# Kernel tuning notes

Measured on AMD Instinct MI355X. Metric: run time of the kernel, lower is better.

## Reference

```python
import jax, jax.numpy as jnp
import numpy as np

INNER = 64  # hardcoded inner_dim in the torch module


def _knn_idx(pos, k):
    # dgcnn-style knn: topk of negative squared distance (includes self)
    d2 = jnp.sum(pos * pos, axis=-1)                      # (b, n)
    sim = 2.0 * jnp.einsum('bic,bjc->bij', pos, pos) - d2[:, :, None] - d2[:, None, :]
    return jax.lax.top_k(sim, k)[1]                       # (b, n, k)


def setup_inputs() -> dict:
    key = jax.random.key(0)
    ks = jax.random.split(key, 16)
    emb_dim = 256
    b, n, k = 8, 2048, 16
    s = 0.05
    inp = {
        'x': jax.random.normal(ks[0], (b, n, emb_dim), dtype=jnp.float32),
        'pos': jax.random.normal(ks[1], (b, n, 3), dtype=jnp.float32),
        'w_qkv': jax.random.normal(ks[2], (emb_dim, 3 * INNER), dtype=jnp.float32) * s,
        'w_pos1': jax.random.normal(ks[3], (3, 64), dtype=jnp.float32) * s,
        'b_pos1': jnp.zeros((64,), dtype=jnp.float32),
        'w_pos2': jax.random.normal(ks[4], (64, INNER), dtype=jnp.float32) * s,
        'b_pos2': jnp.zeros((INNER,), dtype=jnp.float32),
        'w_att1': jax.random.normal(ks[5], (INNER, 4 * INNER), dtype=jnp.float32) * s,
        'b_att1': jnp.zeros((4 * INNER,), dtype=jnp.float32),
        'w_att2': jax.random.normal(ks[6], (4 * INNER, INNER), dtype=jnp.float32) * s,
        'b_att2': jnp.zeros((INNER,), dtype=jnp.float32),
        'w_out': jax.random.normal(ks[7], (INNER, emb_dim), dtype=jnp.float32) * s,
        'b_out': jnp.zeros((emb_dim,), dtype=jnp.float32),
        'k': k,
    }
    return inp


def reference(x, pos, w_qkv, w_pos1, b_pos1, w_pos2, b_pos2,
              w_att1, b_att1, w_att2, b_att2, w_out, b_out, k):
    b, n, _ = x.shape
    qkv = x @ w_qkv                                        # (b, n, 3*INNER)
    q, kk, v = jnp.split(qkv, 3, axis=-1)                  # each (b, n, INNER)

    idx = _knn_idx(pos, k) + (jnp.arange(b) * n)[:, None, None]  # flat offsets
    idxf = idx.reshape(-1)

    def gather(t, d):
        return jnp.take(t.reshape(b * n, d), idxf, axis=0).reshape(b, n, k, d)

    pos_nn = gather(pos, 3)                                # (b, n, k, 3)
    rel_pos = pos_nn - pos[:, :, None, :]
    rpe = jax.nn.relu(rel_pos @ w_pos1 + b_pos1) @ w_pos2 + b_pos2  # (b, n, k, INNER)

    q_nn = gather(q, INNER)
    k_nn = gather(kk, INNER)
    v_nn = gather(v, INNER) + rpe

    h = q_nn - k_nn + rpe
    sim = jax.nn.relu(h @ w_att1 + b_att1) @ w_att2 + b_att2       # (b, n, k, INNER)

    # NOTE: faithful to torch source — softmax over the CHANNEL dim (-1),
    # then L2-normalize over the neighbor dim (-2).
    attn = jax.nn.softmax(sim, axis=-1)
    norm = jnp.sqrt(jnp.sum(attn * attn, axis=-2, keepdims=True))
    attn = attn / jnp.maximum(norm, 1e-12)

    agg = jnp.sum(attn * v_nn, axis=2)                     # (b, n, INNER)
    return agg @ w_out + b_out                             # (b, n, emb_dim)
```

## Files before the change

### kernel.cpp

```cpp
#include <hip/hip_runtime.h>
#include <stdint.h>

typedef __attribute__((ext_vector_type(8))) short bf8v;
typedef __attribute__((ext_vector_type(4))) float f4v;
typedef __attribute__((ext_vector_type(4))) unsigned int u4v;
typedef __attribute__((ext_vector_type(2))) unsigned int u2v;

#define MFMA16(a,b,c) __builtin_amdgcn_mfma_f32_16x16x32_bf16((a),(b),(c),0,0,0)

__device__ __forceinline__ unsigned short f2bf(float f) {
    unsigned u = __float_as_uint(f);
    return (unsigned short)((u + 0x7FFFu + ((u >> 16) & 1u)) >> 16);
}
#define SW(row,k,L) ((row)*(L) + ((k) ^ (((row)&7)<<3)))

#define WS_QMK   0u
#define WS_V     4194304u
#define WS_AGG   8388608u
#define WS_IDX   12582912u
#define WS_W1T   13631488u
#define WS_W2T   13664256u
#define WS_WPT   13697024u
#define WS_WQK   13705216u
#define WS_WOUT  13770752u

__global__ __launch_bounds__(256) void k_prep(
    const float* __restrict__ w_qkv, const float* __restrict__ w_pos2,
    const float* __restrict__ w_att1, const float* __restrict__ w_att2,
    const float* __restrict__ w_out, char* __restrict__ ws)
{
    int t = blockIdx.x * 256 + threadIdx.x;
    unsigned short* w1i = (unsigned short*)(ws + WS_W1T);
    unsigned short* w2i = (unsigned short*)(ws + WS_W2T);
    unsigned short* wpi = (unsigned short*)(ws + WS_WPT);
    unsigned short* wqi = (unsigned short*)(ws + WS_WQK);
    unsigned short* woi = (unsigned short*)(ws + WS_WOUT);
    if (t < 16384) {
        int hid = t >> 6, k = t & 63;
        w1i[hid*64 + (k ^ ((hid&7)<<3))] = f2bf(w_att1[k*256 + hid]);
    } else if (t < 32768) {
        int i = t - 16384; int ch = i >> 8, k = i & 255;
        w2i[ch*256 + (k ^ ((ch&7)<<3))] = f2bf(w_att2[k*64 + ch]);
    } else if (t < 36864) {
        int i = t - 32768; int ch = i >> 6, k = i & 63;
        wpi[ch*64 + (k ^ ((ch&7)<<3))] = f2bf(w_pos2[k*64 + ch]);
    } else if (t < 69632) {
        int i = t - 36864; int col = i >> 8, k = i & 255;
        float val = (col < 64) ? (w_qkv[k*192 + col] - w_qkv[k*192 + 64 + col])
                               : w_qkv[k*192 + 128 + (col - 64)];
        wqi[col*256 + (k ^ ((col&7)<<3))] = f2bf(val);
    } else if (t < 86016) {
        int i = t - 69632; int col = i >> 6, k = i & 63;
        woi[col*64 + (k ^ ((col&7)<<3))] = f2bf(w_out[k*256 + col]);
    }
}

__global__ __launch_bounds__(256) void k_knn(const float* __restrict__ pos,
                                             int* __restrict__ idxo) {
    const int wid = threadIdx.x >> 6, lane = threadIdx.x & 63;
    const int pid = blockIdx.x * 4 + wid;
    const int b = pid >> 11, i = pid & 2047;
    const float* pb = pos + (size_t)b * 2048 * 3;
    float xi = pb[i*3], yi = pb[i*3+1], zi = pb[i*3+2];
    float d2i = xi*xi; d2i = fmaf(yi, yi, d2i); d2i = fmaf(zi, zi, d2i);
    unsigned long long key[32];
#pragma unroll
    for (int m = 0; m < 32; ++m) {
        int j = m * 64 + lane;
        float xj = pb[j*3], yj = pb[j*3+1], zj = pb[j*3+2];
        float d2j = xj*xj; d2j = fmaf(yj, yj, d2j); d2j = fmaf(zj, zj, d2j);
        float dot = xi*xj; dot = fmaf(yi, yj, dot); dot = fmaf(zi, zj, dot);
        float sim = 2.0f*dot - d2i - d2j;
        unsigned u = __float_as_uint(sim);
        unsigned fk = (u & 0x80000000u) ? ~u : (u | 0x80000000u);
        key[m] = ((unsigned long long)fk << 32) | (unsigned)(0xFFFFFFFFu - (unsigned)j);
    }
    unsigned long long lmax = key[0];
#pragma unroll
    for (int m = 1; m < 32; ++m) lmax = (key[m] > lmax) ? key[m] : lmax;
    int my = 0;
    for (int it = 0; it < 16; ++it) {
        unsigned long long wmax = lmax;
#pragma unroll
        for (int st = 32; st >= 1; st >>= 1) {
            unsigned long long o = __shfl_xor(wmax, st);
            wmax = (o > wmax) ? o : wmax;
        }
        int jw = (int)(0xFFFFFFFFu - (unsigned)(wmax & 0xFFFFFFFFull));
        if (lane == it) my = jw;
        if (lmax == wmax) {
#pragma unroll
            for (int m = 0; m < 32; ++m) if (key[m] == wmax) key[m] = 0ull;
            lmax = key[0];
#pragma unroll
            for (int m = 1; m < 32; ++m) lmax = (key[m] > lmax) ? key[m] : lmax;
        }
    }
    if (lane < 16) idxo[pid * 16 + lane] = b * 2048 + my;
}

__global__ __launch_bounds__(256, 1) void k_qkv(const float* __restrict__ x,
        const char* __restrict__ wimg, float* __restrict__ qmk, float* __restrict__ v) {
    extern __shared__ char smem[];
    unsigned short* WQ = (unsigned short*)smem;
    unsigned short* XT = (unsigned short*)(smem + 65536);
    const int tid = threadIdx.x, wid = tid >> 6, lane = tid & 63;
    const int q4 = lane >> 4, l15 = lane & 15;
#pragma unroll
    for (int itn = 0; itn < 16; ++itn) {
        int off = itn * 4096 + tid * 16;
        *(u4v*)(smem + off) = *(const u4v*)(wimg + off);
    }
    __syncthreads();
    {
        int r = tid >> 2, k64 = (tid & 3) * 64;
        const float* xr = x + ((size_t)blockIdx.x * 64 + r) * 256 + k64;
#pragma unroll
        for (int c = 0; c < 8; ++c) {
            f4v a = *(const f4v*)(xr + c*8);
            f4v bq = *(const f4v*)(xr + c*8 + 4);
            bf8v s;
            s[0]=(short)f2bf(a[0]); s[1]=(short)f2bf(a[1]); s[2]=(short)f2bf(a[2]); s[3]=(short)f2bf(a[3]);
            s[4]=(short)f2bf(bq[0]); s[5]=(short)f2bf(bq[1]); s[6]=(short)f2bf(bq[2]); s[7]=(short)f2bf(bq[3]);
            *(bf8v*)&XT[SW(r, k64 + c*8, 256)] = s;
        }
    }
    f4v z = {0.f,0.f,0.f,0.f};
    f4v acc[8];
#pragma unroll
    for (int n = 0; n < 8; ++n) acc[n] = z;
    const int arow = wid*16 + l15;
#pragma unroll
    for (int ks = 0; ks < 8; ++ks) {
        int k0 = ks*32 + q4*8;
        bf8v a = *(const bf8v*)&XT[SW(arow, k0, 256)];
#pragma unroll
        for (int nt = 0; nt < 8; ++nt) {
            bf8v bq = *(const bf8v*)&WQ[SW(nt*16 + l15, k0, 256)];
            acc[nt] = MFMA16(a, bq, acc[nt]);
        }
    }
    size_t rbase = (size_t)blockIdx.x * 64 + wid*16 + q4*4;
#pragma unroll
    for (int nt = 0; nt < 8; ++nt) {
        int col = nt*16 + l15;
#pragma unroll
        for (int j = 0; j < 4; ++j) {
            if (nt < 4) qmk[(rbase + j)*64 + col] = acc[nt][j];
            else        v[(rbase + j)*64 + (col - 64)] = acc[nt][j];
        }
    }
}

__global__ __launch_bounds__(256, 1) void k_att(
    const float* __restrict__ qmk, const float* __restrict__ v,
    const float* __restrict__ pos, const int* __restrict__ idx,
    const float* __restrict__ w_pos1, const float* __restrict__ b_pos1,
    const float* __restrict__ b_pos2, const float* __restrict__ b_att1,
    const float* __restrict__ b_att2, const char* __restrict__ wblob,
    float* __restrict__ agg)
{
    extern __shared__ char smem[];
    unsigned short* W1T = (unsigned short*)smem;
    unsigned short* W2T = (unsigned short*)(smem + 32768);
    unsigned short* WPT = (unsigned short*)(smem + 65536);
    const int tid = threadIdx.x, wid = tid >> 6, lane = tid & 63;
    const int q4 = lane >> 4, l15 = lane & 15;
    char* wb = smem + 73728 + wid * 16640;
    unsigned short* PH = (unsigned short*)wb;
    unsigned short* H  = (unsigned short*)(wb + 2048);
    float*          RV = (float*)(wb + 4096);
    unsigned short* C1 = (unsigned short*)(wb + 8448);

#pragma unroll
    for (int itn = 0; itn < 18; ++itn) {
        int off = itn * 4096 + tid * 16;
        *(u4v*)(smem + off) = *(const u4v*)(wblob + off);
    }
    __syncthreads();

    float bp2[16], ba2[16];
#pragma unroll
    for (int mt = 0; mt < 4; ++mt)
#pragma unroll
        for (int j = 0; j < 4; ++j) {
            int ch = mt*16 + q4*4 + j;
            bp2[mt*4+j] = b_pos2[ch];
            ba2[mt*4+j] = b_att2[ch];
        }

    const int r4 = lane >> 2, c16 = (lane & 3) * 16;
    f4v z = {0.f,0.f,0.f,0.f};

    for (int it = 0; it < 16; ++it) {
        const int point = (blockIdx.x * 4 + wid) * 16 + it;
        {
            int grow = point * 16 + r4;
            int flat = idx[grow];
            float cx = pos[point*3], cy = pos[point*3+1], cz = pos[point*3+2];
            float r0 = pos[flat*3] - cx, r1 = pos[flat*3+1] - cy, r2 = pos[flat*3+2] - cz;
            bf8v lo, hi;
#pragma unroll
            for (int i = 0; i < 16; ++i) {
                int h = c16 + i;
                float t = fmaf(r2, w_pos1[128+h], fmaf(r1, w_pos1[64+h], fmaf(r0, w_pos1[h], b_pos1[h])));
                t = fmaxf(t, 0.f);
                if (i < 8) lo[i] = (short)f2bf(t); else hi[i-8] = (short)f2bf(t);
            }
            *(bf8v*)&PH[SW(r4, c16, 64)] = lo;
            *(bf8v*)&PH[SW(r4, c16+8, 64)] = hi;
        }
        {
            f4v ga[4];
#pragma unroll
            for (int mt = 0; mt < 4; ++mt) ga[mt] = z;
#pragma unroll
            for (int ks = 0; ks < 2; ++ks) {
                int k0 = ks*32 + q4*8;
                bf8v bfr = *(const bf8v*)&PH[SW(l15, k0, 64)];
#pragma unroll
                for (int mt = 0; mt < 4; ++mt)
                    ga[mt] = MFMA16(*(const bf8v*)&WPT[SW(mt*16 + l15, k0, 64)], bfr, ga[mt]);
            }
#pragma unroll
            for (int mt = 0; mt < 4; ++mt) {
                f4v o;
#pragma unroll
                for (int j = 0; j < 4; ++j) o[j] = ga[mt][j] + bp2[mt*4+j];
                *(f4v*)&RV[l15*68 + mt*16 + q4*4] = o;
            }
        }
        {
            int grow = point * 16 + r4;
            int flat = idx[grow];
            f4v rp[4], qk[4];
#pragma unroll
            for (int i = 0; i < 4; ++i) rp[i] = *(const f4v*)&RV[r4*68 + c16 + i*4];
#pragma unroll
            for (int i = 0; i < 4; ++i) qk[i] = *(const f4v*)(qmk + (size_t)flat*64 + c16 + i*4);
            bf8v lo, hi;
#pragma unroll
            for (int i = 0; i < 16; ++i) {
                float hv = rp[i>>2][i&3] + qk[i>>2][i&3];
                if (i < 8) lo[i] = (short)f2bf(hv); else hi[i-8] = (short)f2bf(hv);
            }
            *(bf8v*)&H[SW(r4, c16, 64)] = lo;
            *(bf8v*)&H[SW(r4, c16+8, 64)] = hi;
#pragma unroll
            for (int i = 0; i < 4; ++i) {
                f4v vv = *(const f4v*)(v + (size_t)flat*64 + c16 + i*4);
                f4v o;
#pragma unroll
                for (int j = 0; j < 4; ++j) o[j] = vv[j] + rp[i][j];
                *(f4v*)&RV[r4*68 + c16 + i*4] = o;
            }
        }
        {
            f4v cc[16];
#pragma unroll
            for (int mt = 0; mt < 16; ++mt) cc[mt] = z;
#pragma unroll
            for (int ks = 0; ks < 2; ++ks) {
                int k0 = ks*32 + q4*8;
                bf8v bfr = *(const bf8v*)&H[SW(l15, k0, 64)];
#pragma unroll
                for (int mt = 0; mt < 16; ++mt)
                    cc[mt] = MFMA16(*(const bf8v*)&W1T[SW(mt*16 + l15, k0, 64)], bfr, cc[mt]);
            }
#pragma unroll
            for (int mt = 0; mt < 16; ++mt) {
                f4v ba = *(const f4v*)(b_att1 + mt*16 + q4*4);
                float t0 = fmaxf(cc[mt][0]+ba[0], 0.f), t1 = fmaxf(cc[mt][1]+ba[1], 0.f);
                float t2 = fmaxf(cc[mt][2]+ba[2], 0.f), t3 = fmaxf(cc[mt][3]+ba[3], 0.f);
                u2v pp;
                pp[0] = (unsigned)f2bf(t0) | ((unsigned)f2bf(t1) << 16);
                pp[1] = (unsigned)f2bf(t2) | ((unsigned)f2bf(t3) << 16);
                *(u2v*)&C1[SW(l15, mt*16 + q4*4, 256)] = pp;
            }
        }
        {
            f4v ss[4];
#pragma unroll
            for (int mt = 0; mt < 4; ++mt) ss[mt] = z;
#pragma unroll
            for (int ks = 0; ks < 8; ++ks) {
                int k0 = ks*32 + q4*8;
                bf8v bfr = *(const bf8v*)&C1[SW(l15, k0, 256)];
#pragma unroll
                for (int mt = 0; mt < 4; ++mt)
                    ss[mt] = MFMA16(*(const bf8v*)&W2T[SW(mt*16 + l15, k0, 256)], bfr, ss[mt]);
            }
            float e[16];
            float mx = -3.4e38f;
#pragma unroll
            for (int i = 0; i < 16; ++i) { e[i] = ss[i>>2][i&3] + ba2[i]; mx = fmaxf(mx, e[i]); }
            mx = fmaxf(mx, __shfl_xor(mx, 16));
            mx = fmaxf(mx, __shfl_xor(mx, 32));
            float sum = 0.f;
#pragma unroll
            for (int i = 0; i < 16; ++i) { e[i] = __expf(e[i] - mx); sum += e[i]; }
            sum += __shfl_xor(sum, 16);
            sum += __shfl_xor(sum, 32);
            float inv = 1.0f / sum;
            float nn[16];
#pragma unroll
            for (int i = 0; i < 16; ++i) { e[i] *= inv; nn[i] = e[i]*e[i]; }
#pragma unroll
            for (int st = 1; st <= 8; st <<= 1)
#pragma unroll
                for (int i = 0; i < 16; ++i) nn[i] += __shfl_xor(nn[i], st);
            float ag[16];
#pragma unroll
            for (int mt = 0; mt < 4; ++mt) {
                f4v vn = *(const f4v*)&RV[l15*68 + mt*16 + q4*4];
#pragma unroll
                for (int j = 0; j < 4; ++j) {
                    int i = mt*4 + j;
                    float a = e[i] / fmaxf(sqrtf(nn[i]), 1e-12f);
                    ag[i] = a * vn[j];
                }
            }
#pragma unroll
            for (int st = 1; st <= 8; st <<= 1)
#pragma unroll
                for (int i = 0; i < 16; ++i) ag[i] += __shfl_xor(ag[i], st);
            if (l15 == 0) {
#pragma unroll
                for (int mt = 0; mt < 4; ++mt) {
                    f4v o;
#pragma unroll
                    for (int j = 0; j < 4; ++j) o[j] = ag[mt*4+j];
                    *(f4v*)(agg + (size_t)point*64 + mt*16 + q4*4) = o;
                }
            }
        }
    }
}

__global__ __launch_bounds__(256, 1) void k_out(const float* __restrict__ agg,
        const char* __restrict__ wimg, const float* __restrict__ b_out,
        float* __restrict__ outp) {
    extern __shared__ char smem[];
    unsigned short* WO = (unsigned short*)smem;
    unsigned short* AT = (unsigned short*)(smem + 32768);
    const int tid = threadIdx.x, wid = tid >> 6, lane = tid & 63;
    const int q4 = lane >> 4, l15 = lane & 15;
#pragma unroll
    for (int itn = 0; itn < 8; ++itn) {
        int off = itn * 4096 + tid * 16;
        *(u4v*)(smem + off) = *(const u4v*)(wimg + off);
    }
    __syncthreads();
    {
        int r = tid >> 2, k16 = (tid & 3) * 16;
        const float* ar = agg + ((size_t)blockIdx.x * 64 + r) * 64 + k16;
        bf8v lo, hi;
#pragma unroll
        for (int i = 0; i < 16; ++i) {
            float t = ar[i];
            if (i < 8) lo[i] = (short)f2bf(t); else hi[i-8] = (short)f2bf(t);
        }
        *(bf8v*)&AT[SW(r, k16, 64)] = lo;
        *(bf8v*)&AT[SW(r, k16+8, 64)] = hi;
    }
    f4v z = {0.f,0.f,0.f,0.f};
    f4v acc[16];
#pragma unroll
    for (int nt = 0; nt < 16; ++nt) acc[nt] = z;
#pragma unroll
    for (int ks = 0; ks < 2; ++ks) {
        int k0 = ks*32 + q4*8;
        bf8v a = *(const bf8v*)&AT[SW(wid*16 + l15, k0, 64)];
#pragma unroll
        for (int nt = 0; nt < 16; ++nt) {
            bf8v bq = *(const bf8v*)&WO[SW(nt*16 + l15, k0, 64)];
            acc[nt] = MFMA16(a, bq, acc[nt]);
        }
    }
    size_t rbase = (size_t)blockIdx.x * 64 + wid*16 + q4*4;
#pragma unroll
    for (int nt = 0; nt < 16; ++nt) {
        int col = nt*16 + l15;
        float bo = b_out[col];
#pragma unroll
        for (int j = 0; j < 4; ++j)
            outp[(rbase + j)*256 + col] = acc[nt][j] + bo;
    }
}

extern "C" void kernel_launch(void* const* d_in, const int* in_sizes, int n_in,
                              void* d_out, int out_size, void* d_ws, size_t ws_size,
                              hipStream_t stream) {
    (void)in_sizes; (void)n_in; (void)out_size; (void)ws_size;
    const float* x      = (const float*)d_in[0];
    const float* pos    = (const float*)d_in[1];
    const float* w_qkv  = (const float*)d_in[2];
    const float* w_pos1 = (const float*)d_in[3];
    const float* b_pos1 = (const float*)d_in[4];
    const float* w_pos2 = (const float*)d_in[5];
    const float* b_pos2 = (const float*)d_in[6];
    const float* w_att1 = (const float*)d_in[7];
    const float* b_att1 = (const float*)d_in[8];
    const float* w_att2 = (const float*)d_in[9];
    const float* b_att2 = (const float*)d_in[10];
    const float* w_out  = (const float*)d_in[11];
    const float* b_out  = (const float*)d_in[12];
    float* outp = (float*)d_out;

    char* ws = (char*)d_ws;
    float* qmk = (float*)(ws + WS_QMK);
    float* v   = (float*)(ws + WS_V);
    float* agg = (float*)(ws + WS_AGG);
    int*   idx = (int*)(ws + WS_IDX);

    k_prep<<<dim3(336), dim3(256), 0, stream>>>(w_qkv, w_pos2, w_att1, w_att2, w_out, ws);
    k_knn<<<dim3(4096), dim3(256), 0, stream>>>(pos, idx);
    k_qkv<<<dim3(256), dim3(256), 98304, stream>>>(x, ws + WS_WQK, qmk, v);
    k_att<<<dim3(256), dim3(256), 140288, stream>>>(qmk, v, pos, idx,
                                                    w_pos1, b_pos1, b_pos2, b_att1, b_att2,
                                                    ws + WS_W1T, agg);
    k_out<<<dim3(256), dim3(256), 40960, stream>>>(agg, ws + WS_WOUT, b_out, outp);
}
```

Baseline: 591.8 us.

## Restructure attention kernel to keep rpe/v in registers and use 8 waves per block

```diff
diff --git a/kernel.cpp b/kernel.cpp
--- a/kernel.cpp
+++ b/kernel.cpp
@@ -152,7 +152,7 @@
     }
 }
 
-__global__ __launch_bounds__(256, 1) void k_att(
+__global__ __launch_bounds__(512, 2) void k_att(
     const float* __restrict__ qmk, const float* __restrict__ v,
     const float* __restrict__ pos, const int* __restrict__ idx,
     const float* __restrict__ w_pos1, const float* __restrict__ b_pos1,
@@ -166,172 +166,148 @@
     unsigned short* WPT = (unsigned short*)(smem + 65536);
     const int tid = threadIdx.x, wid = tid >> 6, lane = tid & 63;
     const int q4 = lane >> 4, l15 = lane & 15;
-    char* wb = smem + 73728 + wid * 16640;
+    const int r4 = lane >> 2, c16 = (lane & 3) * 16;
+    char* wb = smem + 73728 + wid * 10240;
+    unsigned short* P  = (unsigned short*)wb;
     unsigned short* PH = (unsigned short*)wb;
-    unsigned short* H  = (unsigned short*)(wb + 2048);
-    float*          RV = (float*)(wb + 4096);
-    unsigned short* C1 = (unsigned short*)(wb + 8448);
-
-#pragma unroll
-    for (int itn = 0; itn < 18; ++itn) {
-        int off = itn * 4096 + tid * 16;
+    unsigned short* H  = (unsigned short*)(wb + 8192);
+
+#pragma unroll
+    for (int it = 0; it < 9; ++it) {
+        int off = it * 8192 + tid * 16;
         *(u4v*)(smem + off) = *(const u4v*)(wblob + off);
     }
     __syncthreads();
 
-    float bp2[16], ba2[16];
-#pragma unroll
-    for (int mt = 0; mt < 4; ++mt)
-#pragma unroll
-        for (int j = 0; j < 4; ++j) {
-            int ch = mt*16 + q4*4 + j;
-            bp2[mt*4+j] = b_pos2[ch];
-            ba2[mt*4+j] = b_att2[ch];
-        }
-
-    const int r4 = lane >> 2, c16 = (lane & 3) * 16;
-    f4v z = {0.f,0.f,0.f,0.f};
-
-    for (int it = 0; it < 16; ++it) {
-        const int point = (blockIdx.x * 4 + wid) * 16 + it;
+#pragma unroll 1
+    for (int g = 0; g < 8; ++g) {
+        const int p = (blockIdx.x * 8 + wid) * 8 + g;
+        const int rowbase = p * 16;
+
+        const int flat_l = idx[rowbase + l15];
+        f4v qk[4], vv[4];
+#pragma unroll
+        for (int mt = 0; mt < 4; ++mt)
+            qk[mt] = *(const f4v*)(qmk + (size_t)flat_l * 64 + mt*16 + q4*4);
+#pragma unroll
+        for (int mt = 0; mt < 4; ++mt)
+            vv[mt] = *(const f4v*)(v + (size_t)flat_l * 64 + mt*16 + q4*4);
+
         {
-            int grow = point * 16 + r4;
-            int flat = idx[grow];
-            float cx = pos[point*3], cy = pos[point*3+1], cz = pos[point*3+2];
-            float r0 = pos[flat*3] - cx, r1 = pos[flat*3+1] - cy, r2 = pos[flat*3+2] - cz;
+            int flat_r = idx[rowbase + r4];
+            float cx = pos[p*3], cy = pos[p*3+1], cz = pos[p*3+2];
+            float r0 = pos[flat_r*3] - cx, r1 = pos[flat_r*3+1] - cy, r2v = pos[flat_r*3+2] - cz;
             bf8v lo, hi;
 #pragma unroll
-            for (int i = 0; i < 16; ++i) {
-                int h = c16 + i;
-                float t = fmaf(r2, w_pos1[128+h], fmaf(r1, w_pos1[64+h], fmaf(r0, w_pos1[h], b_pos1[h])));
-                t = fmaxf(t, 0.f);
-                if (i < 8) lo[i] = (short)f2bf(t); else hi[i-8] = (short)f2bf(t);
+            for (int u = 0; u < 4; ++u) {
+                f4v w0 = *(const f4v*)(w_pos1 + c16 + u*4);
+                f4v w1 = *(const f4v*)(w_pos1 + 64 + c16 + u*4);
+                f4v w2 = *(const f4v*)(w_pos1 + 128 + c16 + u*4);
+                f4v bb = *(const f4v*)(b_pos1 + c16 + u*4);
+#pragma unroll
+                for (int j = 0; j < 4; ++j) {
+                    float t = fmaf(r2v, w2[j], fmaf(r1, w1[j], fmaf(r0, w0[j], bb[j])));
+                    t = fmaxf(t, 0.f);
+                    if (u < 2) lo[u*4+j] = (short)f2bf(t);
+                    else       hi[(u-2)*4+j] = (short)f2bf(t);
+                }
             }
             *(bf8v*)&PH[SW(r4, c16, 64)] = lo;
             *(bf8v*)&PH[SW(r4, c16+8, 64)] = hi;
         }
-        {
-            f4v ga[4];
-#pragma unroll
-            for (int mt = 0; mt < 4; ++mt) ga[mt] = z;
-#pragma unroll
-            for (int ks = 0; ks < 2; ++ks) {
-                int k0 = ks*32 + q4*8;
-                bf8v bfr = *(const bf8v*)&PH[SW(l15, k0, 64)];
-#pragma unroll
-                for (int mt = 0; mt < 4; ++mt)
-                    ga[mt] = MFMA16(*(const bf8v*)&WPT[SW(mt*16 + l15, k0, 64)], bfr, ga[mt]);
+
+        f4v rp[4];
+#pragma unroll
+        for (int mt = 0; mt < 4; ++mt) rp[mt] = *(const f4v*)(b_pos2 + mt*16 + q4*4);
+#pragma unroll
+        for (int ks = 0; ks < 2; ++ks) {
+            int k0 = ks*32 + q4*8;
+            bf8v bfr = *(const bf8v*)&PH[SW(l15, k0, 64)];
+#pragma unroll
+            for (int mt = 0; mt < 4; ++mt)
+                rp[mt] = MFMA16(*(const bf8v*)&WPT[SW(mt*16+l15, k0, 64)], bfr, rp[mt]);
+        }
+
+        f4v vn[4];
+#pragma unroll
+        for (int mt = 0; mt < 4; ++mt) {
+            float h0 = rp[mt][0] + qk[mt][0], h1 = rp[mt][1] + qk[mt][1];
+            float h2 = rp[mt][2] + qk[mt][2], h3 = rp[mt][3] + qk[mt][3];
+            u2v pp;
+            pp[0] = (unsigned)f2bf(h0) | ((unsigned)f2bf(h1) << 16);
+            pp[1] = (unsigned)f2bf(h2) | ((unsigned)f2bf(h3) << 16);
+            *(u2v*)&H[SW(l15, mt*16 + q4*4, 64)] = pp;
+            vn[mt] = rp[mt] + vv[mt];
+        }
+
+        f4v c1[16];
+#pragma unroll
+        for (int mt = 0; mt < 16; ++mt) c1[mt] = *(const f4v*)(b_att1 + mt*16 + q4*4);
+#pragma unroll
+        for (int ks = 0; ks < 2; ++ks) {
+            int k0 = ks*32 + q4*8;
+            bf8v bfr = *(const bf8v*)&H[SW(l15, k0, 64)];
+#pragma unroll
+            for (int mt = 0; mt < 16; ++mt)
+                c1[mt] = MFMA16(*(const bf8v*)&W1T[SW(mt*16+l15, k0, 64)], bfr, c1[mt]);
+        }
+
+#pragma unroll
+        for (int mt = 0; mt < 16; ++mt) {
+            float t0 = fmaxf(c1[mt][0], 0.f), t1 = fmaxf(c1[mt][1], 0.f);
+            float t2 = fmaxf(c1[mt][2], 0.f), t3 = fmaxf(c1[mt][3], 0.f);
+            u2v pp;
+            pp[0] = (unsigned)f2bf(t0) | ((unsigned)f2bf(t1) << 16);
+            pp[1] = (unsigned)f2bf(t2) | ((unsigned)f2bf(t3) << 16);
+            *(u2v*)&P[SW(l15, mt*16 + q4*4, 256)] = pp;
+        }
+
+        f4v ss[4];
+#pragma unroll
+        for (int mt = 0; mt < 4; ++mt) ss[mt] = *(const f4v*)(b_att2 + mt*16 + q4*4);
+#pragma unroll
+        for (int ks = 0; ks < 8; ++ks) {
+            int k0 = ks*32 + q4*8;
+            bf8v bfr = *(const bf8v*)&P[SW(l15, k0, 256)];
+#pragma unroll
+            for (int mt = 0; mt < 4; ++mt)
+                ss[mt] = MFMA16(*(const bf8v*)&W2T[SW(mt*16+l15, k0, 256)], bfr, ss[mt]);
+        }
+
+        float e[16]; float mx = -3.4e38f;
+#pragma unroll
+        for (int i = 0; i < 16; ++i) { e[i] = ss[i>>2][i&3]; mx = fmaxf(mx, e[i]); }
+        mx = fmaxf(mx, __shfl_xor(mx, 16));
+        mx = fmaxf(mx, __shfl_xor(mx, 32));
+        float sum = 0.f;
+#pragma unroll
+        for (int i = 0; i < 16; ++i) { e[i] = __expf(e[i] - mx); sum += e[i]; }
+        sum += __shfl_xor(sum, 16);
+        sum += __shfl_xor(sum, 32);
+        float inv = 1.0f / sum;
+        float nn[16], av[16];
+#pragma unroll
+        for (int i = 0; i < 16; ++i) {
+            e[i] *= inv;
+            nn[i] = e[i] * e[i];
+            av[i] = e[i] * vn[i>>2][i&3];
+        }
+#pragma unroll
+        for (int st = 1; st <= 8; st <<= 1) {
+#pragma unroll
+            for (int i = 0; i < 16; ++i) {
+                nn[i] += __shfl_xor(nn[i], st);
+                av[i] += __shfl_xor(av[i], st);
             }
+        }
+        if (l15 == 0) {
 #pragma unroll
             for (int mt = 0; mt < 4; ++mt) {
                 f4v o;
 #pragma unroll
-                for (int j = 0; j < 4; ++j) o[j] = ga[mt][j] + bp2[mt*4+j];
-                *(f4v*)&RV[l15*68 + mt*16 + q4*4] = o;
-            }
-        }
-        {
-            int grow = point * 16 + r4;
-            int flat = idx[grow];
-            f4v rp[4], qk[4];
-#pragma unroll
-            for (int i = 0; i < 4; ++i) rp[i] = *(const f4v*)&RV[r4*68 + c16 + i*4];
-#pragma unroll
-            for (int i = 0; i < 4; ++i) qk[i] = *(const f4v*)(qmk + (size_t)flat*64 + c16 + i*4);
-            bf8v lo, hi;
-#pragma unroll
-            for (int i = 0; i < 16; ++i) {
-                float hv = rp[i>>2][i&3] + qk[i>>2][i&3];
-                if (i < 8) lo[i] = (short)f2bf(hv); else hi[i-8] = (short)f2bf(hv);
-            }
-            *(bf8v*)&H[SW(r4, c16, 64)] = lo;
-            *(bf8v*)&H[SW(r4, c16+8, 64)] = hi;
-#pragma unroll
-            for (int i = 0; i < 4; ++i) {
-                f4v vv = *(const f4v*)(v + (size_t)flat*64 + c16 + i*4);
-                f4v o;
-#pragma unroll
-                for (int j = 0; j < 4; ++j) o[j] = vv[j] + rp[i][j];
-                *(f4v*)&RV[r4*68 + c16 + i*4] = o;
-            }
-        }
-        {
-            f4v cc[16];
-#pragma unroll
-            for (int mt = 0; mt < 16; ++mt) cc[mt] = z;
-#pragma unroll
-            for (int ks = 0; ks < 2; ++ks) {
-                int k0 = ks*32 + q4*8;
-                bf8v bfr = *(const bf8v*)&H[SW(l15, k0, 64)];
-#pragma unroll
-                for (int mt = 0; mt < 16; ++mt)
-                    cc[mt] = MFMA16(*(const bf8v*)&W1T[SW(mt*16 + l15, k0, 64)], bfr, cc[mt]);
-            }
-#pragma unroll
-            for (int mt = 0; mt < 16; ++mt) {
-                f4v ba = *(const f4v*)(b_att1 + mt*16 + q4*4);
-                float t0 = fmaxf(cc[mt][0]+ba[0], 0.f), t1 = fmaxf(cc[mt][1]+ba[1], 0.f);
-                float t2 = fmaxf(cc[mt][2]+ba[2], 0.f), t3 = fmaxf(cc[mt][3]+ba[3], 0.f);
-                u2v pp;
-                pp[0] = (unsigned)f2bf(t0) | ((unsigned)f2bf(t1) << 16);
-                pp[1] = (unsigned)f2bf(t2) | ((unsigned)f2bf(t3) << 16);
-                *(u2v*)&C1[SW(l15, mt*16 + q4*4, 256)] = pp;
-            }
-        }
-        {
-            f4v ss[4];
-#pragma unroll
-            for (int mt = 0; mt < 4; ++mt) ss[mt] = z;
-#pragma unroll
-            for (int ks = 0; ks < 8; ++ks) {
-                int k0 = ks*32 + q4*8;
-                bf8v bfr = *(const bf8v*)&C1[SW(l15, k0, 256)];
-#pragma unroll
-                for (int mt = 0; mt < 4; ++mt)
-                    ss[mt] = MFMA16(*(const bf8v*)&W2T[SW(mt*16 + l15, k0, 256)], bfr, ss[mt]);
-            }
-            float e[16];
-            float mx = -3.4e38f;
-#pragma unroll
-            for (int i = 0; i < 16; ++i) { e[i] = ss[i>>2][i&3] + ba2[i]; mx = fmaxf(mx, e[i]); }
-            mx = fmaxf(mx, __shfl_xor(mx, 16));
-            mx = fmaxf(mx, __shfl_xor(mx, 32));
-            float sum = 0.f;
-#pragma unroll
-            for (int i = 0; i < 16; ++i) { e[i] = __expf(e[i] - mx); sum += e[i]; }
-            sum += __shfl_xor(sum, 16);
-            sum += __shfl_xor(sum, 32);
-            float inv = 1.0f / sum;
-            float nn[16];
-#pragma unroll
-            for (int i = 0; i < 16; ++i) { e[i] *= inv; nn[i] = e[i]*e[i]; }
-#pragma unroll
-            for (int st = 1; st <= 8; st <<= 1)
-#pragma unroll
-                for (int i = 0; i < 16; ++i) nn[i] += __shfl_xor(nn[i], st);
-            float ag[16];
-#pragma unroll
-            for (int mt = 0; mt < 4; ++mt) {
-                f4v vn = *(const f4v*)&RV[l15*68 + mt*16 + q4*4];
-#pragma unroll
-                for (int j = 0; j < 4; ++j) {
-                    int i = mt*4 + j;
-                    float a = e[i] / fmaxf(sqrtf(nn[i]), 1e-12f);
-                    ag[i] = a * vn[j];
-                }
-            }
-#pragma unroll
-            for (int st = 1; st <= 8; st <<= 1)
-#pragma unroll
-                for (int i = 0; i < 16; ++i) ag[i] += __shfl_xor(ag[i], st);
-            if (l15 == 0) {
-#pragma unroll
-                for (int mt = 0; mt < 4; ++mt) {
-                    f4v o;
-#pragma unroll
-                    for (int j = 0; j < 4; ++j) o[j] = ag[mt*4+j];
-                    *(f4v*)(agg + (size_t)point*64 + mt*16 + q4*4) = o;
-                }
+                for (int j = 0; j < 4; ++j)
+                    o[j] = av[mt*4+j] / fmaxf(sqrtf(nn[mt*4+j]), 1e-12f);
+                *(f4v*)(agg + (size_t)p*64 + mt*16 + q4*4) = o;
             }
         }
     }
@@ -416,7 +392,7 @@
     k_prep<<<dim3(336), dim3(256), 0, stream>>>(w_qkv, w_pos2, w_att1, w_att2, w_out, ws);
     k_knn<<<dim3(4096), dim3(256), 0, stream>>>(pos, idx);
     k_qkv<<<dim3(256), dim3(256), 98304, stream>>>(x, ws + WS_WQK, qmk, v);
-    k_att<<<dim3(256), dim3(256), 140288, stream>>>(qmk, v, pos, idx,
+    k_att<<<dim3(256), dim3(512), 155648, stream>>>(qmk, v, pos, idx,
                                                     w_pos1, b_pos1, b_pos2, b_att1, b_att2,
                                                     ws + WS_W1T, agg);
     k_out<<<dim3(256), dim3(256), 40960, stream>>>(agg, ws + WS_WOUT, b_out, outp);
```

New measurement: 581.6 us. No clear change (-1.7%).
